# Performance work log

Measured on AMD Instinct MI355X. Metric: run time of the kernel, lower is better.

The kernel has to match this reference:

```python
import jax, jax.numpy as jnp
import numpy as np

EPS = 1e-5  # torch InstanceNorm2d default eps


def _unfold3x3(x):
    # x: [B, C, H, W] -> [B, C, 9, H, W] (3x3 patches, zero pad=1, stride=1)
    B, C, H, W = x.shape
    xp = jnp.pad(x, ((0, 0), (0, 0), (1, 1), (1, 1)))
    return jnp.stack([xp[:, :, i:i + H, j:j + W]
                      for i in range(3) for j in range(3)], axis=2)


def _instance_norm(x):
    # InstanceNorm2d(affine=False): per-(sample, channel) spatial normalization
    m = x.mean(axis=(2, 3), keepdims=True)
    v = x.var(axis=(2, 3), keepdims=True)
    return (x - m) * jax.lax.rsqrt(v + EPS)


def setup_inputs() -> dict:
    key = jax.random.key(0)
    k1, k2, k3, k4, k5 = jax.random.split(key, 5)
    B, C, O, H, W = 8, 256, 128, 64, 64
    feat = jax.random.normal(k1, (B, C, H, W), dtype=jnp.float32)
    # scale guide so the Gaussian adaptive kernel exp(-0.5*||dg||^2) over 256
    # channels is non-degenerate (not ~delta at center)
    guide = jax.random.normal(k2, (B, C, H, W), dtype=jnp.float32) * 0.05
    pac_w = jax.random.normal(k3, (C, C, 3, 3), dtype=jnp.float32) * 0.02
    dec_w = jax.random.normal(k4, (O, C, 3, 3), dtype=jnp.float32) * 0.02
    dec_b = jax.random.normal(k5, (O,), dtype=jnp.float32) * 0.02
    return {"feat": feat, "guide": guide, "pac_w": pac_w,
            "dec_w": dec_w, "dec_b": dec_b}


def reference(feat, guide, pac_w, dec_w, dec_b):
    # --- PacConv2d: pixel-adaptive conv with fixed Gaussian guide kernel ---
    gu = _unfold3x3(guide)                      # [B,Cg,9,H,W]
    dg = gu - guide[:, :, None]                 # diff to center pixel
    kern = jnp.exp(-0.5 * jnp.sum(dg * dg, axis=1, keepdims=True))  # [B,1,9,H,W]
    xu = _unfold3x3(feat)                       # [B,C,9,H,W]
    O = pac_w.shape[0]
    pac_out = jnp.einsum('bckhw,ock->bohw', xu * kern,
                         pac_w.reshape(O, -1, 9))  # [B,C,H,W]
    # --- InstanceNorm + ReLU ---
    feat2 = jax.nn.relu(_instance_norm(pac_out))
    # --- decoding: Conv2d(3x3, pad=1) + InstanceNorm + ReLU ---
    y = jax.lax.conv_general_dilated(feat2, dec_w, window_strides=(1, 1),
                                     padding='SAME')
    y = y + dec_b[None, :, None, None]
    return jax.nn.relu(_instance_norm(y))
```

## Files before the change

kernel.cpp:

```cpp
#include <hip/hip_runtime.h>
#include <hip/hip_bf16.h>
#include <hip/hip_fp16.h>

#define IN_EPS 1e-5f

typedef __attribute__((ext_vector_type(8))) short short8;
typedef __attribute__((ext_vector_type(4))) float f32x4;
typedef _Float16 half8 __attribute__((ext_vector_type(8)));

__device__ __forceinline__ short f2h(float f) {
  __half h = __float2half(f);
  return *(short*)&h;
}
__device__ __forceinline__ float h2f(short s) {
  __half h = *(__half*)&s;
  return __half2float(h);
}

__device__ __forceinline__ short8 pkmul(short8 v, unsigned kbits) {
  union { short8 s; unsigned u[4]; } x;
  x.s = v;
  __half2 k = *(__half2*)&kbits;
#pragma unroll
  for (int i = 0; i < 4; ++i) {
    __half2 h = *(__half2*)&x.u[i];
    h = __hmul2(h, k);
    x.u[i] = *(unsigned*)&h;
  }
  return x.s;
}

__global__ void wconv_k(const float* __restrict__ src, short* __restrict__ dst,
                        int O) {
  int idx = blockIdx.x * 256 + threadIdx.x;
  if (idx >= O * 2304) return;
  int o = idx / 2304;
  int r = idx - o * 2304;
  int c = r / 9;
  int k = r - c * 9;
  int mblk = o >> 7, ol = o & 127, cb = c >> 6, cl = c & 63;
  dst[(((size_t)(mblk * 36 + cb * 9 + k)) << 13) + (ol << 6) + (cl ^ ((ol & 7) << 3))]
      = f2h(src[idx]);
}

__global__ __launch_bounds__(256) void kern_k(const float* __restrict__ g,
                                              float* __restrict__ kern) {
  int h = blockIdx.x, b = blockIdx.y;
  int t = threadIdx.x, w = t & 63, cg = t >> 6;
  float acc[9];
#pragma unroll
  for (int k = 0; k < 9; ++k) acc[k] = 0.f;
  const float* base = g + (((size_t)b * 256 + (cg << 6)) << 12) + (h << 6) + w;
#pragma unroll 4
  for (int cc = 0; cc < 64; ++cc) {
    const float* gp = base + ((size_t)cc << 12);
    float mid = gp[0];
    float top = (h > 0) ? gp[-64] : 0.f;
    float bot = (h < 63) ? gp[64] : 0.f;
    float rows[3] = {top, mid, bot};
#pragma unroll
    for (int i = 0; i < 3; ++i) {
      float v = rows[i];
      float l = __shfl_up(v, 1);
      float r = __shfl_down(v, 1);
      if (w == 0) l = 0.f;
      if (w == 63) r = 0.f;
      float dl = l - mid, dm = v - mid, dr = r - mid;
      acc[i * 3 + 0] += dl * dl;
      acc[i * 3 + 1] += dm * dm;
      acc[i * 3 + 2] += dr * dr;
    }
  }
  __shared__ float red[4][9][64];
#pragma unroll
  for (int k = 0; k < 9; ++k) red[cg][k][w] = acc[k];
  __syncthreads();
  for (int idx = t; idx < 576; idx += 256) {
    int k = idx >> 6, w2 = idx & 63;
    float s = red[0][k][w2] + red[1][k][w2] + red[2][k][w2] + red[3][k][w2];
    kern[(((size_t)b * 9 + k) << 12) + (h << 6) + w2] = expf(-0.5f * s);
  }
}

template <int MTOT, bool USE_KERN, bool USE_NORM, bool KSPLIT, bool XF16>
__global__ __launch_bounds__(512, 4) void gemm_conv(
    const short* __restrict__ Wimg, const void* __restrict__ Xv,
    const float* __restrict__ Kf, const float* __restrict__ MRin,
    short* __restrict__ outA, short* __restrict__ outB) {
  __shared__ short ldsA[2][8192];
  __shared__ short ldsB[16384];
  __shared__ short ldsS[512];
  __shared__ short klds[USE_KERN ? 1152 : 1];

  const int t = threadIdx.x;
  const int nblk = blockIdx.x, b = blockIdx.z;
  const int mblk = KSPLIT ? 0 : blockIdx.y;
  const int cb0 = KSPLIT ? (int)blockIdx.y * 2 : 0;
  const int ncb = KSPLIT ? 2 : 4;
  short* __restrict__ outp = (KSPLIT && blockIdx.y) ? outB : outA;
  const int h0 = nblk * 2;
  const int lane = t & 63, wid = t >> 6;
  const int wr = wid >> 2, wc = wid & 3;
  const int fr = lane & 15, kg = (lane >> 4) << 3;
  const int scol = t & 63, c8 = (t >> 6) << 3;

  f32x4 acc[4][2];
#pragma unroll
  for (int i = 0; i < 4; ++i)
#pragma unroll
    for (int j = 0; j < 2; ++j) acc[i][j] = {0.f, 0.f, 0.f, 0.f};

  float breg[4][8];
  float2 mreg[8];

  auto loadA = [&](int pan, short8* ar) {
    const short* src =
        Wimg + (((size_t)(mblk * 36 + cb0 * 9 + pan)) << 13) + (t << 3);
    ar[0] = *(const short8*)(src);
    ar[1] = *(const short8*)(src + 4096);
  };
  auto writeA = [&](const short8* ar, int buf) {
    *(short8*)&ldsA[buf][t << 3] = ar[0];
    *(short8*)&ldsA[buf][4096 + (t << 3)] = ar[1];
  };
  auto loadBregs = [&](int cbrel) {
    int c0 = ((cb0 + cbrel) << 6) + c8;
    size_t off = (((size_t)b * 256 + c0) << 12) + scol;
    if (USE_NORM) {
#pragma unroll
      for (int i = 0; i < 8; ++i)
        mreg[i] = ((const float2*)MRin)[b * 256 + c0 + i];
    }
#pragma unroll
    for (int r = 0; r < 4; ++r) {
      int hr = h0 - 1 + r;
      bool okr = (unsigned)hr < 64u;
#pragma unroll
      for (int i = 0; i < 8; ++i) {
        if (XF16) {
          const short* src = (const short*)Xv + off + (hr << 6);
          breg[r][i] = okr ? h2f(src[(size_t)i << 12]) : 0.f;
        } else {
          const float* src = (const float*)Xv + off + (hr << 6);
          breg[r][i] = okr ? src[(size_t)i << 12] : 0.f;
        }
      }
    }
  };
  auto writeB = [&]() {
#pragma unroll
    for (int r = 0; r < 4; ++r) {
      short8 pk;
#pragma unroll
      for (int i = 0; i < 8; ++i) {
        float x = breg[r][i];
        if (USE_NORM) x = fmaxf((x - mreg[i].x) * mreg[i].y, 0.f);
        pk[i] = f2h(x);
      }
      *(short8*)&ldsB[(((r << 6) + scol) << 6) + (c8 ^ ((scol & 7) << 3))] = pk;
    }
  };
  auto computeTap = [&](int tap, int buf) {
    const int di = tap / 3 - 1, dj = tap % 3 - 1;
    unsigned kq2[2];
    if (USE_KERN) {
#pragma unroll
      for (int nf = 0; nf < 2; ++nf) {
        short kh = klds[tap * 128 + (wc << 5) + (nf << 4) + fr];
        __half h = *(__half*)&kh;
        __half2 h2 = __half2half2(h);
        kq2[nf] = *(unsigned*)&h2;
      }
    }
#pragma unroll
    for (int ks = 0; ks < 2; ++ks) {
      int kb = (ks << 5) + kg;
      short8 a4[4], b2[2];
#pragma unroll
      for (int mf = 0; mf < 4; ++mf) {
        int rr = (wr << 6) + (mf << 4) + fr;
        a4[mf] = *(const short8*)&ldsA[buf][(rr << 6) + (kb ^ ((rr & 7) << 3))];
      }
#pragma unroll
      for (int nf = 0; nf < 2; ++nf) {
        int px = (wc << 5) + (nf << 4) + fr;
        int rr2 = (px >> 6) + di + 1;
        int wcol = (px & 63) + dj;
        int kbs = kb ^ ((wcol & 7) << 3);
        const short* pm = &ldsB[(((rr2 << 6) + wcol) << 6) + kbs];
        const short* ps = &ldsS[(((rr2 << 1) + (wcol == 64)) << 6) + kbs];
        short8 bb = *(const short8*)(((unsigned)wcol < 64u) ? pm : ps);
        if (USE_KERN) bb = pkmul(bb, kq2[nf]);
        b2[nf] = bb;
      }
      __builtin_amdgcn_s_setprio(1);
#pragma unroll
      for (int mf = 0; mf < 4; ++mf)
#pragma unroll
        for (int nf = 0; nf < 2; ++nf)
          acc[mf][nf] = __builtin_amdgcn_mfma_f32_16x16x32_f16(
              *(half8*)&a4[mf], *(half8*)&b2[nf], acc[mf][nf], 0, 0, 0);
      __builtin_amdgcn_s_setprio(0);
    }
  };

  if (t < 64) {
    short8 z = {0, 0, 0, 0, 0, 0, 0, 0};
    *(short8*)&ldsS[t << 3] = z;
  }
  if (USE_KERN) {
    for (int idx = t; idx < 1152; idx += 512) {
      int tap = idx >> 7, px = idx & 127;
      klds[idx] = f2h(Kf[(((size_t)b * 9 + tap) << 12) +
                         ((h0 + (px >> 6)) << 6) + (px & 63)]);
    }
  }
  {
    short8 ar[2];
    loadA(0, ar);
    loadBregs(0);
    writeA(ar, 0);
    writeB();
  }
  __syncthreads();

  const int nt = ncb * 9;
  int tap = 0, cbrel = 0;
  for (int pan = 0; pan < nt; ++pan) {
    int buf = pan & 1;
    bool more = (pan + 1) < nt;
    bool lastTap = (tap == 8);
    short8 ar[2];
    if (more) loadA(pan + 1, ar);
    if (USE_KERN && more && lastTap) loadBregs(cbrel + 1);
    computeTap(tap, buf);
    if (more && lastTap) {
      __syncthreads();
      if (!USE_NORM) {
        writeB();
      } else {
        loadBregs(cbrel + 1);
        writeB();
      }
      writeA(ar, buf ^ 1);
      __syncthreads();
    } else if (more) {
      writeA(ar, buf ^ 1);
      __syncthreads();
    }
    if (++tap == 9) { tap = 0; ++cbrel; }
  }

  const int row4 = (lane >> 4) << 2;
#pragma unroll
  for (int mf = 0; mf < 4; ++mf) {
    int o = (mblk << 7) + (wr << 6) + (mf << 4) + row4;
    size_t ob = (((size_t)b * MTOT + o) << 12) + (nblk << 7) + (wc << 5) + fr;
#pragma unroll
    for (int nf = 0; nf < 2; ++nf) {
      f32x4 v = acc[mf][nf];
      size_t oo = ob + (nf << 4);
      outp[oo] = f2h(v[0]);
      outp[oo + 4096] = f2h(v[1]);
      outp[oo + 8192] = f2h(v[2]);
      outp[oo + 12288] = f2h(v[3]);
    }
  }
}

__global__ __launch_bounds__(256) void reduce_mv(const short* __restrict__ x,
                                                 float* __restrict__ mr) {
  int bc = blockIdx.x, t = threadIdx.x;
  const short8* xp = (const short8*)(x + ((size_t)bc << 12));
  float s = 0.f, s2 = 0.f;
  for (int i = t; i < 512; i += 256) {
    short8 v = xp[i];
#pragma unroll
    for (int j = 0; j < 8; ++j) {
      float f = h2f(v[j]);
      s += f;
      s2 += f * f;
    }
  }
#pragma unroll
  for (int off = 32; off; off >>= 1) {
    s += __shfl_down(s, off);
    s2 += __shfl_down(s2, off);
  }
  __shared__ float ls[4], ls2[4];
  int wid = t >> 6, lane = t & 63;
  if (!lane) { ls[wid] = s; ls2[wid] = s2; }
  __syncthreads();
  if (!t) {
    s = ls[0] + ls[1] + ls[2] + ls[3];
    s2 = ls2[0] + ls2[1] + ls2[2] + ls2[3];
    float m = s * (1.f / 4096.f);
    float var = s2 * (1.f / 4096.f) - m * m;
    mr[2 * bc] = m;
    mr[2 * bc + 1] = rsqrtf(fmaxf(var, 0.f) + IN_EPS);
  }
}

__global__ __launch_bounds__(256) void reduce_mv2(const short* __restrict__ xa,
                                                  const short* __restrict__ xb,
                                                  float* __restrict__ mr) {
  int bc = blockIdx.x, t = threadIdx.x;
  const short8* ap = (const short8*)(xa + ((size_t)bc << 12));
  const short8* bp = (const short8*)(xb + ((size_t)bc << 12));
  float s = 0.f, s2 = 0.f;
  for (int i = t; i < 512; i += 256) {
    short8 va = ap[i], vb = bp[i];
#pragma unroll
    for (int j = 0; j < 8; ++j) {
      float f = h2f(va[j]) + h2f(vb[j]);
      s += f;
      s2 += f * f;
    }
  }
#pragma unroll
  for (int off = 32; off; off >>= 1) {
    s += __shfl_down(s, off);
    s2 += __shfl_down(s2, off);
  }
  __shared__ float ls[4], ls2[4];
  int wid = t >> 6, lane = t & 63;
  if (!lane) { ls[wid] = s; ls2[wid] = s2; }
  __syncthreads();
  if (!t) {
    s = ls[0] + ls[1] + ls[2] + ls[3];
    s2 = ls2[0] + ls2[1] + ls2[2] + ls2[3];
    float m = s * (1.f / 4096.f);
    float var = s2 * (1.f / 4096.f) - m * m;
    mr[2 * bc] = m;
    mr[2 * bc + 1] = rsqrtf(fmaxf(var, 0.f) + IN_EPS);
  }
}

__global__ __launch_bounds__(256) void finalize2(const short* __restrict__ ya,
                                                 const short* __restrict__ yb,
                                                 const float* __restrict__ mr,
                                                 float* __restrict__ out) {
  int i = blockIdx.x * 256 + threadIdx.x;
  int bc = i >> 9;
  float m = mr[2 * bc], r = mr[2 * bc + 1];
  short8 va = ((const short8*)ya)[i];
  short8 vb = ((const short8*)yb)[i];
  float4 o0, o1;
#pragma unroll
  for (int j = 0; j < 8; ++j) {
    float f = fmaxf((h2f(va[j]) + h2f(vb[j]) - m) * r, 0.f);
    if (j < 4) ((float*)&o0)[j] = f;
    else ((float*)&o1)[j - 4] = f;
  }
  ((float4*)out)[2 * i] = o0;
  ((float4*)out)[2 * i + 1] = o1;
}

extern "C" void kernel_launch(void* const* d_in, const int* in_sizes, int n_in,
                              void* d_out, int out_size, void* d_ws,
                              size_t ws_size, hipStream_t stream) {
  (void)in_sizes; (void)n_in; (void)out_size; (void)ws_size;
  const float* feat  = (const float*)d_in[0];
  const float* guide = (const float*)d_in[1];
  const float* pac_w = (const float*)d_in[2];
  const float* dec_w = (const float*)d_in[3];
  float* out = (float*)d_out;
  char* ws = (char*)d_ws;

  float* kernbuf = (float*)(ws);
  short* Ws1     = (short*)(ws + 0x120000);
  short* Ws2     = (short*)(ws + 0x240000);
  float* mr1     = (float*)(ws + 0x2D0000);
  float* mr2     = (float*)(ws + 0x2D4000);
  short* pac     = (short*)(ws + 0x300000);
  short* ybufA   = (short*)(ws + 0x1300000);
  short* ybufB   = (short*)(ws + 0x1B00000);

  wconv_k<<<(256 * 2304 + 255) / 256, 256, 0, stream>>>(pac_w, Ws1, 256);
  wconv_k<<<(128 * 2304 + 255) / 256, 256, 0, stream>>>(dec_w, Ws2, 128);
  kern_k<<<dim3(64, 8), 256, 0, stream>>>(guide, kernbuf);

  gemm_conv<256, true, false, false, false><<<dim3(32, 2, 8), 512, 0, stream>>>(
      Ws1, feat, kernbuf, nullptr, pac, nullptr);
  reduce_mv<<<8 * 256, 256, 0, stream>>>(pac, mr1);
  gemm_conv<128, false, true, true, true><<<dim3(32, 2, 8), 512, 0, stream>>>(
      Ws2, pac, nullptr, mr1, ybufA, ybufB);
  reduce_mv2<<<8 * 128, 256, 0, stream>>>(ybufA, ybufB, mr2);
  finalize2<<<2048, 256, 0, stream>>>(ybufA, ybufB, mr2, out);
}
```

Measured before the change: 136.3 us.

## Compute two guide rows per block and prefetch normalized B operand early

The guide-kernel kernel now processes two output rows per 1024-thread block, splitting channels into 16 groups so each loaded row feeds two output rows. This cuts redundant guide loads from 3 to 2 rows per output row. In the second conv GEMM, the next channel block's activations are now prefetched before the tap compute rather than after the barrier, with the mean/rstd loads moved into writeB. The prefetch hides global load latency at the cost of more live registers.

```diff
diff --git a/kernel.cpp b/kernel.cpp
--- a/kernel.cpp
+++ b/kernel.cpp
@@ -43,42 +43,61 @@
       = f2h(src[idx]);
 }
 
-__global__ __launch_bounds__(256) void kern_k(const float* __restrict__ g,
-                                              float* __restrict__ kern) {
-  int h = blockIdx.x, b = blockIdx.y;
+__global__ __launch_bounds__(1024) void kern_k(const float* __restrict__ g,
+                                               float* __restrict__ kern) {
+  int hb = blockIdx.x, b = blockIdx.y;
+  int h0 = hb * 2;
   int t = threadIdx.x, w = t & 63, cg = t >> 6;
-  float acc[9];
-#pragma unroll
-  for (int k = 0; k < 9; ++k) acc[k] = 0.f;
-  const float* base = g + (((size_t)b * 256 + (cg << 6)) << 12) + (h << 6) + w;
+  float acc[2][9];
+#pragma unroll
+  for (int hh = 0; hh < 2; ++hh)
+#pragma unroll
+    for (int k = 0; k < 9; ++k) acc[hh][k] = 0.f;
+  const float* base = g + (((size_t)b * 256 + (cg << 4)) << 12) + (h0 << 6) + w;
 #pragma unroll 4
-  for (int cc = 0; cc < 64; ++cc) {
+  for (int cc = 0; cc < 16; ++cc) {
     const float* gp = base + ((size_t)cc << 12);
-    float mid = gp[0];
-    float top = (h > 0) ? gp[-64] : 0.f;
-    float bot = (h < 63) ? gp[64] : 0.f;
-    float rows[3] = {top, mid, bot};
-#pragma unroll
-    for (int i = 0; i < 3; ++i) {
+    float r0 = (h0 > 0) ? gp[-64] : 0.f;
+    float r1 = gp[0];
+    float r2 = gp[64];
+    float r3 = (h0 < 62) ? gp[128] : 0.f;
+    float rows[4] = {r0, r1, r2, r3};
+    float ls[4], rs[4];
+#pragma unroll
+    for (int i = 0; i < 4; ++i) {
       float v = rows[i];
       float l = __shfl_up(v, 1);
       float r = __shfl_down(v, 1);
       if (w == 0) l = 0.f;
       if (w == 63) r = 0.f;
-      float dl = l - mid, dm = v - mid, dr = r - mid;
-      acc[i * 3 + 0] += dl * dl;
-      acc[i * 3 + 1] += dm * dm;
-      acc[i * 3 + 2] += dr * dr;
-    }
-  }
-  __shared__ float red[4][9][64];
-#pragma unroll
-  for (int k = 0; k < 9; ++k) red[cg][k][w] = acc[k];
+      ls[i] = l;
+      rs[i] = r;
+    }
+#pragma unroll
+    for (int hh = 0; hh < 2; ++hh) {
+      float ctr = rows[hh + 1];
+#pragma unroll
+      for (int i = 0; i < 3; ++i) {
+        float dl = ls[hh + i] - ctr, dm = rows[hh + i] - ctr, dr = rs[hh + i] - ctr;
+        acc[hh][i * 3 + 0] += dl * dl;
+        acc[hh][i * 3 + 1] += dm * dm;
+        acc[hh][i * 3 + 2] += dr * dr;
+      }
+    }
+  }
+  __shared__ float red[16][2][9][64];
+#pragma unroll
+  for (int hh = 0; hh < 2; ++hh)
+#pragma unroll
+    for (int k = 0; k < 9; ++k) red[cg][hh][k][w] = acc[hh][k];
   __syncthreads();
-  for (int idx = t; idx < 576; idx += 256) {
-    int k = idx >> 6, w2 = idx & 63;
-    float s = red[0][k][w2] + red[1][k][w2] + red[2][k][w2] + red[3][k][w2];
-    kern[(((size_t)b * 9 + k) << 12) + (h << 6) + w2] = expf(-0.5f * s);
+  for (int idx = t; idx < 1152; idx += 1024) {
+    int hh = idx / 576, rem = idx - hh * 576;
+    int k = rem >> 6, w2 = rem & 63;
+    float s = 0.f;
+#pragma unroll
+    for (int gi = 0; gi < 16; ++gi) s += red[gi][hh][k][w2];
+    kern[(((size_t)b * 9 + k) << 12) + ((h0 + hh) << 6) + w2] = expf(-0.5f * s);
   }
 }
 
@@ -111,7 +130,6 @@
     for (int j = 0; j < 2; ++j) acc[i][j] = {0.f, 0.f, 0.f, 0.f};
 
   float breg[4][8];
-  float2 mreg[8];
 
   auto loadA = [&](int pan, short8* ar) {
     const short* src =
@@ -126,11 +144,6 @@
   auto loadBregs = [&](int cbrel) {
     int c0 = ((cb0 + cbrel) << 6) + c8;
     size_t off = (((size_t)b * 256 + c0) << 12) + scol;
-    if (USE_NORM) {
-#pragma unroll
-      for (int i = 0; i < 8; ++i)
-        mreg[i] = ((const float2*)MRin)[b * 256 + c0 + i];
-    }
 #pragma unroll
     for (int r = 0; r < 4; ++r) {
       int hr = h0 - 1 + r;
@@ -147,7 +160,14 @@
       }
     }
   };
-  auto writeB = [&]() {
+  auto writeB = [&](int cbrel) {
+    float2 mreg[8];
+    if (USE_NORM) {
+      int c0 = ((cb0 + cbrel) << 6) + c8;
+#pragma unroll
+      for (int i = 0; i < 8; ++i)
+        mreg[i] = ((const float2*)MRin)[b * 256 + c0 + i];
+    }
 #pragma unroll
     for (int r = 0; r < 4; ++r) {
       short8 pk;
@@ -220,7 +240,7 @@
     loadA(0, ar);
     loadBregs(0);
     writeA(ar, 0);
-    writeB();
+    writeB(0);
   }
   __syncthreads();
 
@@ -232,16 +252,11 @@
     bool lastTap = (tap == 8);
     short8 ar[2];
     if (more) loadA(pan + 1, ar);
-    if (USE_KERN && more && lastTap) loadBregs(cbrel + 1);
+    if (more && lastTap) loadBregs(cbrel + 1);
     computeTap(tap, buf);
     if (more && lastTap) {
       __syncthreads();
-      if (!USE_NORM) {
-        writeB();
-      } else {
-        loadBregs(cbrel + 1);
-        writeB();
-      }
+      writeB(cbrel + 1);
       writeA(ar, buf ^ 1);
       __syncthreads();
     } else if (more) {
@@ -378,7 +393,7 @@
 
   wconv_k<<<(256 * 2304 + 255) / 256, 256, 0, stream>>>(pac_w, Ws1, 256);
   wconv_k<<<(128 * 2304 + 255) / 256, 256, 0, stream>>>(dec_w, Ws2, 128);
-  kern_k<<<dim3(64, 8), 256, 0, stream>>>(guide, kernbuf);
+  kern_k<<<dim3(32, 8), 1024, 0, stream>>>(guide, kernbuf);
 
   gemm_conv<256, true, false, false, false><<<dim3(32, 2, 8), 512, 0, stream>>>(
       Ws1, feat, kernbuf, nullptr, pac, nullptr);
```

New measurement: 121.7 us (median of 2 runs). 10.7% less time.
